# Kernel tuning notes

Measured on AMD Instinct MI355X. Metric: run time of the kernel, lower is better.

Reference implementation:

```python
import jax, jax.numpy as jnp
import numpy as np

N_NODES = 50000
N_EDGES = 800000
D_IN = 64
D_OUT = 64


def setup_inputs() -> dict:
    key = jax.random.key(0)
    k1, k2, k3, k4, k5 = jax.random.split(key, 5)
    features = jax.random.normal(k1, (N_NODES, D_IN), dtype=jnp.float32)
    edge_src = jax.random.randint(k2, (N_EDGES,), 0, N_NODES, dtype=jnp.int32)
    edge_dst = jax.random.randint(k3, (N_EDGES,), 0, N_NODES, dtype=jnp.int32)
    edge_weight = jax.random.uniform(k4, (N_EDGES,), dtype=jnp.float32)
    # Linear(2*D_IN, D_OUT): weight [D_OUT, 2*D_IN], bias [D_OUT]
    W = jax.random.normal(k5, (D_OUT, 2 * D_IN), dtype=jnp.float32) * (1.0 / np.sqrt(2 * D_IN))
    b = jnp.zeros((D_OUT,), dtype=jnp.float32)
    return {"features": features, "edge_src": edge_src, "edge_dst": edge_dst,
            "edge_weight": edge_weight, "W": W, "b": b}


def reference(features, edge_src, edge_dst, edge_weight, W, b):
    n = features.shape[0]
    # spmm(adj, features): out[i] = sum_j adj[i,j] * features[j]
    gathered = features[edge_src] * edge_weight[:, None]          # [E, D_IN]
    neighbor = jax.ops.segment_sum(gathered, edge_dst, num_segments=n)  # [N, D_IN]
    combined = jnp.concatenate([features, neighbor], axis=1)     # [N, 2*D_IN]
    out = combined @ W.T + b                                      # [N, D_OUT]
    # F.normalize(p=2, dim=1): x / max(||x||, 1e-12)
    norm = jnp.maximum(jnp.linalg.norm(out, axis=1, keepdims=True), 1e-12)
    return out / norm
```

## Files before the change

kernel.cpp:

```cpp
#include <hip/hip_runtime.h>

#define D 64
#define TILE 1024
#define RB 8
#define EPB 2048
#define EPT 8

__device__ __forceinline__ float rlane(float v, int l) {
    return __int_as_float(__builtin_amdgcn_readlane(__float_as_int(v), l));
}

__global__ __launch_bounds__(256) void hist_kernel(
    const int* __restrict__ edge_dst, int* __restrict__ deg,
    int n_edges, int n_nodes)
{
    __shared__ int s_cnt;
    __shared__ int s_d[EPB];
    int r = blockIdx.x & (RB - 1);
    int chunk = blockIdx.x >> 3;
    int lo = (int)((long long)r * n_nodes / RB);
    int hi = (int)((long long)(r + 1) * n_nodes / RB);
    if (threadIdx.x == 0) s_cnt = 0;
    __syncthreads();

    int base = chunk * EPB + threadIdx.x * EPT;
    int d[EPT];
    if (base + EPT - 1 < n_edges) {
        int4 v0 = *(const int4*)(edge_dst + base);
        int4 v1 = *(const int4*)(edge_dst + base + 4);
        d[0]=v0.x; d[1]=v0.y; d[2]=v0.z; d[3]=v0.w;
        d[4]=v1.x; d[5]=v1.y; d[6]=v1.z; d[7]=v1.w;
    } else {
        #pragma unroll
        for (int k = 0; k < EPT; ++k)
            d[k] = (base + k < n_edges) ? edge_dst[base + k] : -1;
    }

    int lane = threadIdx.x & 63;
    unsigned long long lt = (lane == 63) ? ~0ull >> 1
                                         : ((1ull << (lane + 1)) - 1) >> 1;
    #pragma unroll
    for (int k = 0; k < EPT; ++k) {
        bool m = (d[k] >= lo && d[k] < hi);
        unsigned long long bal = __ballot(m);
        int cw = __popcll(bal);
        if (cw) {
            int bs = 0;
            if (lane == 0) bs = atomicAdd(&s_cnt, cw);
            bs = __builtin_amdgcn_readfirstlane(bs);
            if (m) s_d[bs + __popcll(bal & lt)] = d[k];
        }
    }
    __syncthreads();
    int c = s_cnt;
    for (int i = threadIdx.x; i < c; i += 256) atomicAdd(&deg[s_d[i]], 1);
}

__global__ __launch_bounds__(256) void tile_sum_kernel(
    const int* __restrict__ deg, int* __restrict__ partial, int n)
{
    int t = threadIdx.x;
    int base = blockIdx.x * TILE + t * 4;
    int s = 0;
    if (base + 3 < n) {
        int4 v = *(const int4*)(deg + base);
        s = v.x + v.y + v.z + v.w;
    } else {
        for (int k = 0; k < 4; ++k) if (base + k < n) s += deg[base + k];
    }
    #pragma unroll
    for (int off = 1; off < 64; off <<= 1) s += __shfl_xor(s, off, 64);
    __shared__ int wsum[4];
    int lane = t & 63, wv = t >> 6;
    if (lane == 0) wsum[wv] = s;
    __syncthreads();
    if (t == 0) partial[blockIdx.x] = wsum[0] + wsum[1] + wsum[2] + wsum[3];
}

__global__ __launch_bounds__(64) void scan_partial_kernel(
    const int* __restrict__ partial, int* __restrict__ ppref, int nb,
    int* __restrict__ offsets, int n, int n_edges)
{
    int lane = threadIdx.x;
    int carry = 0;
    for (int base = 0; base < nb; base += 64) {
        int idx = base + lane;
        int v = (idx < nb) ? partial[idx] : 0;
        int inc = v;
        #pragma unroll
        for (int off = 1; off < 64; off <<= 1) {
            int u = __shfl_up(inc, off, 64);
            if (lane >= off) inc += u;
        }
        if (idx < nb) ppref[idx] = carry + inc - v;
        carry += __shfl(inc, 63, 64);
    }
    if (lane == 0) offsets[n] = n_edges;
}

__global__ __launch_bounds__(256) void scan_tile_kernel(
    const int* __restrict__ deg, const int* __restrict__ ppref,
    int* __restrict__ offsets, int* __restrict__ cursor, int n)
{
    int t = threadIdx.x;
    int base = blockIdx.x * TILE + t * 4;
    int e0 = 0, e1 = 0, e2 = 0, e3 = 0;
    if (base + 3 < n) {
        int4 v = *(const int4*)(deg + base);
        e0 = v.x; e1 = v.y; e2 = v.z; e3 = v.w;
    } else {
        if (base + 0 < n) e0 = deg[base + 0];
        if (base + 1 < n) e1 = deg[base + 1];
        if (base + 2 < n) e2 = deg[base + 2];
        if (base + 3 < n) e3 = deg[base + 3];
    }
    int s = e0 + e1 + e2 + e3;
    int inc = s;
    int lane = t & 63, wv = t >> 6;
    #pragma unroll
    for (int off = 1; off < 64; off <<= 1) {
        int u = __shfl_up(inc, off, 64);
        if (lane >= off) inc += u;
    }
    __shared__ int wsum[4];
    if (lane == 63) wsum[wv] = inc;
    __syncthreads();
    int wpre = 0;
    for (int wq = 0; wq < wv; ++wq) wpre += wsum[wq];
    int excl = ppref[blockIdx.x] + wpre + inc - s;
    int o0 = excl, o1 = o0 + e0, o2 = o1 + e1, o3 = o2 + e2;
    if (base + 0 < n) { offsets[base + 0] = o0; cursor[base + 0] = o0; }
    if (base + 1 < n) { offsets[base + 1] = o1; cursor[base + 1] = o1; }
    if (base + 2 < n) { offsets[base + 2] = o2; cursor[base + 2] = o2; }
    if (base + 3 < n) { offsets[base + 3] = o3; cursor[base + 3] = o3; }
}

__global__ __launch_bounds__(256) void fill_kernel(
    const int* __restrict__ edge_src, const int* __restrict__ edge_dst,
    const float* __restrict__ edge_weight,
    int* __restrict__ cursor, int2* __restrict__ csr_sw,
    int n_edges, int n_nodes)
{
    __shared__ int s_cnt;
    __shared__ int s_d[EPB];
    __shared__ int s_e[EPB];
    int r = blockIdx.x & (RB - 1);
    int chunk = blockIdx.x >> 3;
    int lo = (int)((long long)r * n_nodes / RB);
    int hi = (int)((long long)(r + 1) * n_nodes / RB);
    if (threadIdx.x == 0) s_cnt = 0;
    __syncthreads();

    int base = chunk * EPB + threadIdx.x * EPT;
    int d[EPT];
    if (base + EPT - 1 < n_edges) {
        int4 v0 = *(const int4*)(edge_dst + base);
        int4 v1 = *(const int4*)(edge_dst + base + 4);
        d[0]=v0.x; d[1]=v0.y; d[2]=v0.z; d[3]=v0.w;
        d[4]=v1.x; d[5]=v1.y; d[6]=v1.z; d[7]=v1.w;
    } else {
        #pragma unroll
        for (int k = 0; k < EPT; ++k)
            d[k] = (base + k < n_edges) ? edge_dst[base + k] : -1;
    }

    int lane = threadIdx.x & 63;
    unsigned long long lt = (lane == 63) ? ~0ull >> 1
                                         : ((1ull << (lane + 1)) - 1) >> 1;
    #pragma unroll
    for (int k = 0; k < EPT; ++k) {
        bool m = (d[k] >= lo && d[k] < hi);
        unsigned long long bal = __ballot(m);
        int cw = __popcll(bal);
        if (cw) {
            int bs = 0;
            if (lane == 0) bs = atomicAdd(&s_cnt, cw);
            bs = __builtin_amdgcn_readfirstlane(bs);
            if (m) {
                int p = bs + __popcll(bal & lt);
                s_d[p] = d[k];
                s_e[p] = base + k;
            }
        }
    }
    __syncthreads();
    int c = s_cnt;
    for (int i = threadIdx.x; i < c; i += 256) {
        int dk = s_d[i];
        int e  = s_e[i];
        int pos = atomicAdd(&cursor[dk], 1);
        csr_sw[pos] = make_int2(edge_src[e], __float_as_int(edge_weight[e]));
    }
}

__global__ __launch_bounds__(256) void gather_kernel(
    const float* __restrict__ features, const int2* __restrict__ csr_sw,
    const int* __restrict__ offsets, float* __restrict__ neighbor, int n_nodes)
{
    int lane = threadIdx.x & 63;
    int gw = (blockIdx.x * 256 + threadIdx.x) >> 6;
    int nw = (gridDim.x * 256) >> 6;
    for (int i = gw; i < n_nodes; i += nw) {
        int beg = __builtin_amdgcn_readfirstlane(offsets[i]);
        int end = __builtin_amdgcn_readfirstlane(offsets[i + 1]);
        float acc = 0.f;
        int j = beg;
        for (; j + 7 < end; j += 8) {
            int2 p[8];
            float a[8];
            #pragma unroll
            for (int q = 0; q < 8; ++q) p[q] = csr_sw[j + q];
            #pragma unroll
            for (int q = 0; q < 8; ++q)
                a[q] = features[(size_t)p[q].x * D + lane];
            #pragma unroll
            for (int q = 0; q < 8; ++q)
                acc = fmaf(__int_as_float(p[q].y), a[q], acc);
        }
        for (; j < end; ++j) {
            int2 p = csr_sw[j];
            acc = fmaf(__int_as_float(p.y), features[(size_t)p.x * D + lane], acc);
        }
        neighbor[(size_t)i * D + lane] = acc;
    }
}

__global__ __launch_bounds__(256) void gemm_norm_kernel(
    const float* __restrict__ features, const float* __restrict__ neighbor,
    const float* __restrict__ W, const float* __restrict__ bias,
    float* __restrict__ out, int n_nodes)
{
    int lane = threadIdx.x & 63;
    float wr[128];
    const float4* Wv = (const float4*)(W + (size_t)lane * 128);
    #pragma unroll
    for (int q = 0; q < 32; ++q) {
        float4 v = Wv[q];
        wr[4 * q + 0] = v.x; wr[4 * q + 1] = v.y;
        wr[4 * q + 2] = v.z; wr[4 * q + 3] = v.w;
    }
    float bl = bias[lane];

    int gw = (blockIdx.x * 256 + threadIdx.x) >> 6;
    int nw = (gridDim.x * 256) >> 6;
    for (int i = gw; i < n_nodes; i += nw) {
        float cf = features[(size_t)i * D + lane];
        float cn = neighbor[(size_t)i * D + lane];
        float a0 = bl, a1 = 0.f, a2 = 0.f, a3 = 0.f;
        #pragma unroll
        for (int k = 0; k < 32; ++k) {
            a0 = fmaf(rlane(cf, k),      wr[k],      a0);
            a1 = fmaf(rlane(cf, k + 32), wr[k + 32], a1);
            a2 = fmaf(rlane(cn, k),      wr[k + 64], a2);
            a3 = fmaf(rlane(cn, k + 32), wr[k + 96], a3);
        }
        float acc = (a0 + a1) + (a2 + a3);
        float s = acc * acc;
        #pragma unroll
        for (int m = 1; m < 64; m <<= 1) s += __shfl_xor(s, m, 64);
        out[(size_t)i * D + lane] = acc / fmaxf(sqrtf(s), 1e-12f);
    }
}

extern "C" void kernel_launch(void* const* d_in, const int* in_sizes, int n_in,
                              void* d_out, int out_size, void* d_ws, size_t ws_size,
                              hipStream_t stream) {
    const float* features    = (const float*)d_in[0];
    const int*   edge_src    = (const int*)d_in[1];
    const int*   edge_dst    = (const int*)d_in[2];
    const float* edge_weight = (const float*)d_in[3];
    const float* W           = (const float*)d_in[4];
    const float* b           = (const float*)d_in[5];
    float*       out         = (float*)d_out;

    int n = in_sizes[0] / D;
    int E = in_sizes[1];
    int nb = (n + TILE - 1) / TILE;
    int nchunks = (E + EPB - 1) / EPB;

    char* ws = (char*)d_ws;
    auto al = [](size_t x) { return (x + 255) & ~(size_t)255; };
    size_t o = 0;
    int* deg      = (int*)(ws + o); o += al((size_t)n * 4);
    int* cursor   = (int*)(ws + o); o += al((size_t)n * 4);
    int* offsets  = (int*)(ws + o); o += al((size_t)(n + 1) * 4);
    int* partial  = (int*)(ws + o); o += al((size_t)nb * 4);
    int* ppref    = (int*)(ws + o); o += al((size_t)nb * 4);
    int2* csr_sw  = (int2*)(ws + o); o += al((size_t)E * 8);
    float* neighbor = (float*)(ws + o);

    hipMemsetAsync(deg, 0, (size_t)n * 4, stream);

    hist_kernel<<<nchunks * RB, 256, 0, stream>>>(edge_dst, deg, E, n);
    tile_sum_kernel<<<nb, 256, 0, stream>>>(deg, partial, n);
    scan_partial_kernel<<<1, 64, 0, stream>>>(partial, ppref, nb, offsets, n, E);
    scan_tile_kernel<<<nb, 256, 0, stream>>>(deg, ppref, offsets, cursor, n);
    fill_kernel<<<nchunks * RB, 256, 0, stream>>>(edge_src, edge_dst, edge_weight,
                                                  cursor, csr_sw, E, n);
    gather_kernel<<<2048, 256, 0, stream>>>(features, csr_sw, offsets,
                                            neighbor, n);
    gemm_norm_kernel<<<2048, 256, 0, stream>>>(features, neighbor, W, b, out, n);
}
```

Before: 230.4 us.

## Stage W in shared memory and process eight nodes per wave in GEMM

The GEMM+normalize kernel now loads the transposed weight matrix into LDS as float4 instead of holding 128 weights per lane in registers. Each wave computes eight nodes at once, so every weight fetch is reused across eight rows. The launch grid is resized so each node group is handled exactly once, replacing the grid-stride loop. This cuts register pressure and per-row weight traffic, but each block now pays for its own W load into LDS and the number of readlane operations stays the same.

```diff
diff --git a/kernel.cpp b/kernel.cpp
--- a/kernel.cpp
+++ b/kernel.cpp
@@ -230,35 +230,66 @@
     const float* __restrict__ W, const float* __restrict__ bias,
     float* __restrict__ out, int n_nodes)
 {
-    int lane = threadIdx.x & 63;
-    float wr[128];
-    const float4* Wv = (const float4*)(W + (size_t)lane * 128);
-    #pragma unroll
-    for (int q = 0; q < 32; ++q) {
-        float4 v = Wv[q];
-        wr[4 * q + 0] = v.x; wr[4 * q + 1] = v.y;
-        wr[4 * q + 2] = v.z; wr[4 * q + 3] = v.w;
-    }
+    __shared__ float4 Wt4[32][64];
+    int tid = threadIdx.x;
+    #pragma unroll
+    for (int idx = tid; idx < 32 * 64; idx += 256) {
+        int k4 = idx >> 6, o = idx & 63;
+        Wt4[k4][o] = *(const float4*)(W + (size_t)o * 128 + k4 * 4);
+    }
+    __syncthreads();
+
+    int lane = tid & 63;
+    int wv = tid >> 6;
     float bl = bias[lane];
 
-    int gw = (blockIdx.x * 256 + threadIdx.x) >> 6;
-    int nw = (gridDim.x * 256) >> 6;
-    for (int i = gw; i < n_nodes; i += nw) {
-        float cf = features[(size_t)i * D + lane];
-        float cn = neighbor[(size_t)i * D + lane];
-        float a0 = bl, a1 = 0.f, a2 = 0.f, a3 = 0.f;
-        #pragma unroll
-        for (int k = 0; k < 32; ++k) {
-            a0 = fmaf(rlane(cf, k),      wr[k],      a0);
-            a1 = fmaf(rlane(cf, k + 32), wr[k + 32], a1);
-            a2 = fmaf(rlane(cn, k),      wr[k + 64], a2);
-            a3 = fmaf(rlane(cn, k + 32), wr[k + 96], a3);
-        }
-        float acc = (a0 + a1) + (a2 + a3);
-        float s = acc * acc;
-        #pragma unroll
-        for (int m = 1; m < 64; m <<= 1) s += __shfl_xor(s, m, 64);
-        out[(size_t)i * D + lane] = acc / fmaxf(sqrtf(s), 1e-12f);
+    int g = blockIdx.x * 4 + wv;
+    int i0 = g * 8;
+    if (i0 >= n_nodes) return;
+    int cnt = min(8, n_nodes - i0);
+
+    float cf[8], cn[8], acc[8];
+    #pragma unroll
+    for (int t = 0; t < 8; ++t) {
+        int i = i0 + ((t < cnt) ? t : 0);
+        cf[t] = features[(size_t)i * D + lane];
+        cn[t] = neighbor[(size_t)i * D + lane];
+        acc[t] = bl;
+    }
+
+    #pragma unroll 4
+    for (int k4 = 0; k4 < 16; ++k4) {
+        float4 w4 = Wt4[k4][lane];
+        int kb = 4 * k4;
+        #pragma unroll
+        for (int t = 0; t < 8; ++t) {
+            acc[t] = fmaf(rlane(cf[t], kb + 0), w4.x, acc[t]);
+            acc[t] = fmaf(rlane(cf[t], kb + 1), w4.y, acc[t]);
+            acc[t] = fmaf(rlane(cf[t], kb + 2), w4.z, acc[t]);
+            acc[t] = fmaf(rlane(cf[t], kb + 3), w4.w, acc[t]);
+        }
+    }
+    #pragma unroll 4
+    for (int k4 = 16; k4 < 32; ++k4) {
+        float4 w4 = Wt4[k4][lane];
+        int kb = 4 * k4 - 64;
+        #pragma unroll
+        for (int t = 0; t < 8; ++t) {
+            acc[t] = fmaf(rlane(cn[t], kb + 0), w4.x, acc[t]);
+            acc[t] = fmaf(rlane(cn[t], kb + 1), w4.y, acc[t]);
+            acc[t] = fmaf(rlane(cn[t], kb + 2), w4.z, acc[t]);
+            acc[t] = fmaf(rlane(cn[t], kb + 3), w4.w, acc[t]);
+        }
+    }
+
+    #pragma unroll
+    for (int t = 0; t < 8; ++t) {
+        if (t < cnt) {
+            float s = acc[t] * acc[t];
+            #pragma unroll
+            for (int m = 1; m < 64; m <<= 1) s += __shfl_xor(s, m, 64);
+            out[(size_t)(i0 + t) * D + lane] = acc[t] / fmaxf(sqrtf(s), 1e-12f);
+        }
     }
 }
 
@@ -299,5 +330,7 @@
                                                   cursor, csr_sw, E, n);
     gather_kernel<<<2048, 256, 0, stream>>>(features, csr_sw, offsets,
                                             neighbor, n);
-    gemm_norm_kernel<<<2048, 256, 0, stream>>>(features, neighbor, W, b, out, n);
-}
+    int groups = (n + 7) / 8;
+    gemm_norm_kernel<<<(groups + 3) / 4, 256, 0, stream>>>(features, neighbor,
+                                                           W, b, out, n);
+}
```

Result: no change. 230.0 us (-0.1%).
